# Performance work log

Hardware: AMD Instinct MI355X
Metric: run time of the kernel (lower is better)

The kernel has to match this reference:

```python
import jax, jax.numpy as jnp
import numpy as np

D_MODEL = 2048
D_HEAD = 128
NUM_HEADS = 16
D_LATENT = 512
B, S = 4, 2048


def setup_inputs() -> dict:
    key = jax.random.key(0)
    ks = jax.random.split(key, 11)
    sc = lambda fan_in: 1.0 / np.sqrt(fan_in)
    x = jax.random.normal(ks[0], (B, S, D_MODEL), dtype=jnp.float32)
    # weights stored as [in, out] (transpose of torch nn.Linear.weight)
    W_down = jax.random.uniform(ks[1], (D_MODEL, D_LATENT), jnp.float32, -sc(D_MODEL), sc(D_MODEL))
    b_down = jax.random.uniform(ks[2], (D_LATENT,), jnp.float32, -sc(D_MODEL), sc(D_MODEL))
    W_uk = jax.random.uniform(ks[3], (D_LATENT, D_MODEL), jnp.float32, -sc(D_LATENT), sc(D_LATENT))
    b_uk = jax.random.uniform(ks[4], (D_MODEL,), jnp.float32, -sc(D_LATENT), sc(D_LATENT))
    W_uv = jax.random.uniform(ks[5], (D_LATENT, D_MODEL), jnp.float32, -sc(D_LATENT), sc(D_LATENT))
    b_uv = jax.random.uniform(ks[6], (D_MODEL,), jnp.float32, -sc(D_LATENT), sc(D_LATENT))
    W_q = jax.random.uniform(ks[7], (D_MODEL, NUM_HEADS * D_HEAD), jnp.float32, -sc(D_MODEL), sc(D_MODEL))
    b_q = jax.random.uniform(ks[8], (NUM_HEADS * D_HEAD,), jnp.float32, -sc(D_MODEL), sc(D_MODEL))
    W_o = jax.random.uniform(ks[9], (NUM_HEADS * D_HEAD, D_MODEL), jnp.float32, -sc(NUM_HEADS * D_HEAD), sc(NUM_HEADS * D_HEAD))
    b_o = jax.random.uniform(ks[10], (D_MODEL,), jnp.float32, -sc(NUM_HEADS * D_HEAD), sc(NUM_HEADS * D_HEAD))
    return {"x": x, "W_down": W_down, "b_down": b_down, "W_uk": W_uk, "b_uk": b_uk,
            "W_uv": W_uv, "b_uv": b_uv, "W_q": W_q, "b_q": b_q, "W_o": W_o, "b_o": b_o}


def reference(x, W_down, b_down, W_uk, b_uk, W_uv, b_uv, W_q, b_q, W_o, b_o):
    b, s, _ = x.shape
    latents = x @ W_down + b_down                      # [B,S,L]
    keys = latents @ W_uk + b_uk                       # [B,S,D]
    values = latents @ W_uv + b_uv                     # [B,S,D]
    q = (x @ W_q + b_q).reshape(b, s, NUM_HEADS, D_HEAD).transpose(0, 2, 1, 3)
    k = keys.reshape(b, s, NUM_HEADS, D_HEAD).transpose(0, 2, 1, 3)
    v = values.reshape(b, s, NUM_HEADS, D_HEAD).transpose(0, 2, 1, 3)
    scores = jnp.einsum('bhqd,bhkd->bhqk', q, k) / np.sqrt(D_HEAD).astype(np.float32)
    attn = jax.nn.softmax(scores, axis=-1)
    ctx = jnp.einsum('bhqk,bhkd->bhqd', attn, v)       # [B,H,S,Dh]
    ctx = ctx.transpose(0, 2, 1, 3).reshape(b, s, NUM_HEADS * D_HEAD)
    return ctx @ W_o + b_o
```

## Files before the change

kernel.cpp:

```cpp
#include <hip/hip_runtime.h>

#define D_MODEL 2048
#define D_LATENT 512
#define NUM_HEADS 16
#define D_HEAD 128
#define BATCH 4
#define SEQ 2048
#define MTOK (BATCH*SEQ)

typedef __bf16 bf16_t;
typedef __bf16 bf16x4 __attribute__((ext_vector_type(4)));
typedef __bf16 bf16x8 __attribute__((ext_vector_type(8)));
typedef float  f32x4  __attribute__((ext_vector_type(4)));

__device__ __forceinline__ void load_lds16(const bf16_t* g, bf16_t* l) {
  __builtin_amdgcn_global_load_lds(
      (const __attribute__((address_space(1))) void*)g,
      (__attribute__((address_space(3))) void*)l,
      16, 0, 0);
}

__global__ void convert_f32_bf16_kernel(const float* __restrict__ src,
                                        bf16_t* __restrict__ dst, int n4) {
  int i = blockIdx.x * 256 + threadIdx.x;
  if (i >= n4) return;
  float4 v = *(const float4*)&src[(size_t)i * 4];
  bf16x4 o = { (bf16_t)v.x, (bf16_t)v.y, (bf16_t)v.z, (bf16_t)v.w };
  *(bf16x4*)&dst[(size_t)i * 4] = o;
}

__global__ void transpose_w_kernel(const float* __restrict__ src, bf16_t* __restrict__ dst,
                                   int R, int C) {
  __shared__ __align__(16) bf16_t tile[64][66];
  int rt = blockIdx.y * 64, ct = blockIdx.x * 64;
  int lc = threadIdx.x & 63, lr = threadIdx.x >> 6;
  for (int i = 0; i < 64; i += 4)
    tile[lr + i][lc] = (bf16_t)src[(size_t)(rt + lr + i) * C + ct + lc];
  __syncthreads();
  for (int i = 0; i < 64; i += 4)
    dst[(size_t)(ct + lr + i) * R + rt + lc] = tile[lc][lr + i];
}

__global__ void transpose_v_kernel(const bf16_t* __restrict__ v, bf16_t* __restrict__ vt) {
  __shared__ __align__(16) bf16_t tile[64][66];
  int bh = blockIdx.z; int b = bh >> 4, h = bh & 15;
  int st = blockIdx.x * 64, dt = blockIdx.y * 64;
  int lc = threadIdx.x & 63, lr = threadIdx.x >> 6;
  const bf16_t* src = v + (size_t)b * SEQ * D_MODEL + h * D_HEAD;
  for (int i = 0; i < 64; i += 4)
    tile[lr + i][lc] = src[(size_t)(st + lr + i) * D_MODEL + dt + lc];
  __syncthreads();
  bf16_t* dst = vt + (size_t)bh * D_HEAD * SEQ;
  for (int i = 0; i < 64; i += 4)
    dst[(size_t)(dt + lr + i) * SEQ + st + lc] = tile[lc][lr + i];
}

template<typename OutT>
__global__ __launch_bounds__(256, 2) void gemm_bt_kernel(
    const bf16_t* __restrict__ A, const bf16_t* __restrict__ Wt,
    const float* __restrict__ bias, OutT* __restrict__ C,
    int M, int N, int K, float premul)
{
  __shared__ __align__(16) bf16_t As[128 * 32];
  __shared__ __align__(16) bf16_t Bs[128 * 32];
  int tid = threadIdx.x;
  int lane = tid & 63, wave = tid >> 6;
  int wr = (wave >> 1) * 64, wc = (wave & 1) * 64;
  size_t row0 = (size_t)blockIdx.x * 128, col0 = (size_t)blockIdx.y * 128;
  int lr = lane & 15, quad = lane >> 4, rq = quad * 4;

  f32x4 acc[4][4] = {};

  int srow = wave * 32 + (lane >> 2);
  int scol = ((lane & 3) ^ ((lane >> 3) & 3)) * 8;
  const bf16_t* Ag = A  + (row0 + srow) * K + scol;
  const bf16_t* Bg = Wt + (col0 + srow) * K + scol;
  bf16_t* Asw = As + wave * 1024;
  bf16_t* Bsw = Bs + wave * 1024;

  int rchunk = (quad ^ ((lr >> 1) & 3)) * 8;

  for (int k0 = 0; k0 < K; k0 += 32) {
    __syncthreads();
    load_lds16(Ag,          Asw);
    load_lds16(Ag + 16 * K, Asw + 512);
    load_lds16(Bg,          Bsw);
    load_lds16(Bg + 16 * K, Bsw + 512);
    Ag += 32; Bg += 32;
    __syncthreads();

    bf16x8 af[4], bfr[4];
    #pragma unroll
    for (int mi = 0; mi < 4; ++mi)
      af[mi] = *(const bf16x8*)&As[(wr + mi * 16 + lr) * 32 + rchunk];
    #pragma unroll
    for (int ni = 0; ni < 4; ++ni)
      bfr[ni] = *(const bf16x8*)&Bs[(wc + ni * 16 + lr) * 32 + rchunk];
    #pragma unroll
    for (int mi = 0; mi < 4; ++mi)
      #pragma unroll
      for (int ni = 0; ni < 4; ++ni)
        acc[mi][ni] = __builtin_amdgcn_mfma_f32_16x16x32_bf16(af[mi], bfr[ni], acc[mi][ni], 0, 0, 0);
  }

  #pragma unroll
  for (int ni = 0; ni < 4; ++ni) {
    int col = (int)col0 + wc + ni * 16 + lr;
    float bv = bias[col];
    #pragma unroll
    for (int mi = 0; mi < 4; ++mi) {
      #pragma unroll
      for (int r = 0; r < 4; ++r) {
        size_t row = row0 + wr + mi * 16 + rq + r;
        C[row * N + col] = (OutT)((acc[mi][ni][r] + bv) * premul);
      }
    }
  }
}

__global__ __launch_bounds__(256, 2) void attention_kernel(
    const bf16_t* __restrict__ q, const bf16_t* __restrict__ keys,
    const bf16_t* __restrict__ vt, bf16_t* __restrict__ ctx)
{
  __shared__ __align__(16) bf16_t KP[64 * 128];
  __shared__ __align__(16) bf16_t VS[128 * 64];
  int bh = blockIdx.y; int b = bh >> 4, h = bh & 15;
  int qt = blockIdx.x;
  int tid = threadIdx.x, lane = tid & 63, wave = tid >> 6;
  int lr = lane & 15, quad = lane >> 4, kq = quad * 8, rq = quad * 4;
  int l7 = lr & 7;

  const bf16_t* qg = q    + (size_t)(b * SEQ + qt * 128) * D_MODEL + h * D_HEAD;
  const bf16_t* kg = keys + (size_t)b * SEQ * D_MODEL + h * D_HEAD;
  const bf16_t* vg = vt   + (size_t)bh * D_HEAD * SEQ;

  bf16x8 qf[2][4];
  #pragma unroll
  for (int mi = 0; mi < 2; ++mi)
    #pragma unroll
    for (int ks = 0; ks < 4; ++ks)
      qf[mi][ks] = *(const bf16x8*)&qg[(size_t)(wave*32 + mi*16 + lr) * D_MODEL + ks*32 + kq];

  bf16x8 kreg[4], vreg[4];
  const bf16_t* kp4[4];
  const bf16_t* vp4[4];
  bf16_t* kd4[4];
  bf16_t* vd4[4];
  #pragma unroll
  for (int i = 0; i < 4; ++i) {
    int c = tid + i * 256;
    int r = c >> 4, kc = c & 15;
    kp4[i] = kg + (size_t)r * D_MODEL + kc * 8;
    kd4[i] = &KP[r * 128 + ((kc ^ (r & 7)) * 8)];
    int d = c >> 3, vc = c & 7;
    vp4[i] = vg + (size_t)d * SEQ + vc * 8;
    vd4[i] = &VS[d * 64 + ((vc ^ (d & 7)) * 8)];
  }
  #pragma unroll
  for (int i = 0; i < 4; ++i) {
    kreg[i] = *(const bf16x8*)kp4[i];
    vreg[i] = *(const bf16x8*)vp4[i];
  }

  f32x4 accO[2][8] = {};
  float m2[2]   = {-1e30f, -1e30f};
  float lsum[2] = {0.f, 0.f};

  for (int kt = 0; kt < SEQ/64; ++kt) {
    __syncthreads();
    #pragma unroll
    for (int i = 0; i < 4; ++i) {
      *(bf16x8*)kd4[i] = kreg[i];
      *(bf16x8*)vd4[i] = vreg[i];
    }
    __syncthreads();

    f32x4 sc[2][4] = {};
    #pragma unroll
    for (int ks = 0; ks < 4; ++ks) {
      bf16x8 kf[4];
      #pragma unroll
      for (int ni = 0; ni < 4; ++ni)
        kf[ni] = *(const bf16x8*)&KP[(ni*16 + lr) * 128 + (((ks*4 + quad) ^ l7) * 8)];
      __builtin_amdgcn_s_setprio(1);
      #pragma unroll
      for (int mi = 0; mi < 2; ++mi)
        #pragma unroll
        for (int ni = 0; ni < 4; ++ni)
          sc[mi][ni] = __builtin_amdgcn_mfma_f32_16x16x32_bf16(kf[ni], qf[mi][ks], sc[mi][ni], 0, 0, 0);
      __builtin_amdgcn_s_setprio(0);
    }

    __syncthreads();

    if (kt + 1 < SEQ/64) {
      #pragma unroll
      for (int i = 0; i < 4; ++i) {
        kp4[i] += 64 * D_MODEL;
        vp4[i] += 64;
        kreg[i] = *(const bf16x8*)kp4[i];
        vreg[i] = *(const bf16x8*)vp4[i];
      }
    }

    #pragma unroll
    for (int mi = 0; mi < 2; ++mi) {
      float rm = sc[mi][0][0];
      #pragma unroll
      for (int ni = 0; ni < 4; ++ni)
        #pragma unroll
        for (int r = 0; r < 4; ++r) rm = fmaxf(rm, sc[mi][ni][r]);
      rm = fmaxf(rm, __shfl_xor(rm, 16, 64));
      rm = fmaxf(rm, __shfl_xor(rm, 32, 64));

      if (!__all(rm - m2[mi] <= 8.0f)) {
        float mnew  = fmaxf(m2[mi], rm);
        float alpha = exp2f(m2[mi] - mnew);
        m2[mi] = mnew;
        lsum[mi] *= alpha;
        float ar[4];
        #pragma unroll
        for (int r = 0; r < 4; ++r) ar[r] = __shfl(alpha, rq + r, 16);
        #pragma unroll
        for (int nd = 0; nd < 8; ++nd)
          #pragma unroll
          for (int r = 0; r < 4; ++r) accO[mi][nd][r] *= ar[r];
      }

      float rs = 0.f;
      int prow = wave*32 + mi*16 + lr;
      int pbase = prow * 64;
      int psw = prow & 7;
      #pragma unroll
      for (int ni = 0; ni < 4; ++ni) {
        float p0 = exp2f(sc[mi][ni][0] - m2[mi]);
        float p1 = exp2f(sc[mi][ni][1] - m2[mi]);
        float p2 = exp2f(sc[mi][ni][2] - m2[mi]);
        float p3 = exp2f(sc[mi][ni][3] - m2[mi]);
        rs += (p0 + p1) + (p2 + p3);
        bf16x4 pk = { (bf16_t)p0, (bf16_t)p1, (bf16_t)p2, (bf16_t)p3 };
        *(bf16x4*)&KP[pbase + (((ni*2 + (quad>>1)) ^ psw) * 8) + (quad&1)*4] = pk;
      }
      rs += __shfl_xor(rs, 16, 64);
      rs += __shfl_xor(rs, 32, 64);
      lsum[mi] += rs;
    }


    #pragma unroll
    for (int ks2 = 0; ks2 < 2; ++ks2) {
      bf16x8 pf[2], vf[8];
      #pragma unroll
      for (int mi = 0; mi < 2; ++mi)
        pf[mi] = *(const bf16x8*)&KP[(wave*32 + mi*16 + lr) * 64 + (((ks2*4 + quad) ^ l7) * 8)];
      #pragma unroll
      for (int nd = 0; nd < 8; ++nd)
        vf[nd] = *(const bf16x8*)&VS[(nd*16 + lr) * 64 + (((ks2*4 + quad) ^ l7) * 8)];
      __builtin_amdgcn_s_setprio(1);
      #pragma unroll
      for (int mi = 0; mi < 2; ++mi)
        #pragma unroll
        for (int nd = 0; nd < 8; ++nd)
          accO[mi][nd] = __builtin_amdgcn_mfma_f32_16x16x32_bf16(pf[mi], vf[nd], accO[mi][nd], 0, 0, 0);
      __builtin_amdgcn_s_setprio(0);
    }
  }

  bf16_t* og = ctx + (size_t)(b * SEQ + qt * 128) * D_MODEL + h * D_HEAD;
  #pragma unroll
  for (int mi = 0; mi < 2; ++mi) {
    float inv[4];
    #pragma unroll
    for (int r = 0; r < 4; ++r) inv[r] = 1.0f / __shfl(lsum[mi], rq + r, 16);
    #pragma unroll
    for (int r = 0; r < 4; ++r) {
      int row = wave*32 + mi*16 + rq + r;
      #pragma unroll
      for (int nd = 0; nd < 8; ++nd)
        og[(size_t)row * D_MODEL + nd*16 + lr] = (bf16_t)(accO[mi][nd][r] * inv[r]);
    }
  }
}

extern "C" void kernel_launch(void* const* d_in, const int* in_sizes, int n_in,
                              void* d_out, int out_size, void* d_ws, size_t ws_size,
                              hipStream_t stream) {
  const float* x      = (const float*)d_in[0];
  const float* W_down = (const float*)d_in[1];
  const float* b_down = (const float*)d_in[2];
  const float* W_uk   = (const float*)d_in[3];
  const float* b_uk   = (const float*)d_in[4];
  const float* W_uv   = (const float*)d_in[5];
  const float* b_uv   = (const float*)d_in[6];
  const float* W_q    = (const float*)d_in[7];
  const float* b_q    = (const float*)d_in[8];
  const float* W_o    = (const float*)d_in[9];
  const float* b_o    = (const float*)d_in[10];
  float* out = (float*)d_out;

  char* ws = (char*)d_ws;
  bf16_t* xb      = (bf16_t*)ws;  ws += (size_t)MTOK*D_MODEL*2;
  bf16_t* Wt_down = (bf16_t*)ws;  ws += (size_t)D_LATENT*D_MODEL*2;
  bf16_t* Wt_uk   = (bf16_t*)ws;  ws += (size_t)D_MODEL*D_LATENT*2;
  bf16_t* Wt_uv   = (bf16_t*)ws;  ws += (size_t)D_MODEL*D_LATENT*2;
  bf16_t* Wt_q    = (bf16_t*)ws;  ws += (size_t)D_MODEL*D_MODEL*2;
  bf16_t* Wt_o    = (bf16_t*)ws;  ws += (size_t)D_MODEL*D_MODEL*2;
  bf16_t* lat     = (bf16_t*)ws;  ws += (size_t)MTOK*D_LATENT*2;
  bf16_t* keys    = (bf16_t*)ws;  ws += (size_t)MTOK*D_MODEL*2;
  bf16_t* vals    = (bf16_t*)ws;  ws += (size_t)MTOK*D_MODEL*2;
  bf16_t* qm      = (bf16_t*)ws;  ws += (size_t)MTOK*D_MODEL*2;
  bf16_t* vtm     = (bf16_t*)ws;  ws += (size_t)MTOK*D_MODEL*2;
  bf16_t* ctx     = vals;

  const float cs = 0.0883883476483184f * 1.44269504089f;

  convert_f32_bf16_kernel<<<(MTOK*D_MODEL/4 + 255)/256, 256, 0, stream>>>(x, xb, MTOK*D_MODEL/4);

  transpose_w_kernel<<<dim3(D_LATENT/64, D_MODEL/64), 256, 0, stream>>>(W_down, Wt_down, D_MODEL, D_LATENT);
  transpose_w_kernel<<<dim3(D_MODEL/64, D_LATENT/64), 256, 0, stream>>>(W_uk,   Wt_uk,   D_LATENT, D_MODEL);
  transpose_w_kernel<<<dim3(D_MODEL/64, D_LATENT/64), 256, 0, stream>>>(W_uv,   Wt_uv,   D_LATENT, D_MODEL);
  transpose_w_kernel<<<dim3(D_MODEL/64, D_MODEL/64),  256, 0, stream>>>(W_q,    Wt_q,    D_MODEL,  D_MODEL);
  transpose_w_kernel<<<dim3(D_MODEL/64, D_MODEL/64),  256, 0, stream>>>(W_o,    Wt_o,    D_MODEL,  D_MODEL);

  gemm_bt_kernel<bf16_t><<<dim3(MTOK/128, D_LATENT/128), 256, 0, stream>>>(xb,  Wt_down, b_down, lat,  MTOK, D_LATENT, D_MODEL, 1.0f);
  gemm_bt_kernel<bf16_t><<<dim3(MTOK/128, D_MODEL/128),  256, 0, stream>>>(lat, Wt_uk,   b_uk,   keys, MTOK, D_MODEL,  D_LATENT, 1.0f);
  gemm_bt_kernel<bf16_t><<<dim3(MTOK/128, D_MODEL/128),  256, 0, stream>>>(lat, Wt_uv,   b_uv,   vals, MTOK, D_MODEL,  D_LATENT, 1.0f);
  gemm_bt_kernel<bf16_t><<<dim3(MTOK/128, D_MODEL/128),  256, 0, stream>>>(xb,  Wt_q,    b_q,    qm,   MTOK, D_MODEL,  D_MODEL, cs);

  transpose_v_kernel<<<dim3(SEQ/64, D_HEAD/64, BATCH*NUM_HEADS), 256, 0, stream>>>(vals, vtm);

  attention_kernel<<<dim3(SEQ/128, BATCH*NUM_HEADS), 256, 0, stream>>>(qm, keys, vtm, ctx);

  gemm_bt_kernel<float><<<dim3(MTOK/128, D_MODEL/128), 256, 0, stream>>>(ctx, Wt_o, b_o, out, MTOK, D_MODEL, D_MODEL, 1.0f);
}
```

Before: 614.1 us.

## Double-buffer K/V in LDS with separate P buffer and remap attention grid

Attention now keeps two LDS buffers for K and V plus a separate buffer for P. The next tile is stored into the idle buffer during compute, which cuts the per-iteration barriers from three to one. The launch changes to a 1D grid whose index mapping groups heads that share a query tile, presumably to improve cache locality. LDS use per block grows substantially, which could limit occupancy.

After: 601.3 us. -2.1%, faster.

```diff
diff --git a/kernel.cpp b/kernel.cpp
--- a/kernel.cpp
+++ b/kernel.cpp
@@ -122,10 +122,13 @@
     const bf16_t* __restrict__ q, const bf16_t* __restrict__ keys,
     const bf16_t* __restrict__ vt, bf16_t* __restrict__ ctx)
 {
-  __shared__ __align__(16) bf16_t KP[64 * 128];
-  __shared__ __align__(16) bf16_t VS[128 * 64];
-  int bh = blockIdx.y; int b = bh >> 4, h = bh & 15;
-  int qt = blockIdx.x;
+  __shared__ __align__(16) bf16_t KS[2][64 * 128];
+  __shared__ __align__(16) bf16_t VS[2][128 * 64];
+  __shared__ __align__(16) bf16_t PS[128 * 64];
+  int wg = blockIdx.x;
+  int qt = (wg >> 3) & 15;
+  int bh = (wg & 7) | ((wg >> 7) << 3);
+  int b = bh >> 4, h = bh & 15;
   int tid = threadIdx.x, lane = tid & 63, wave = tid >> 6;
   int lr = lane & 15, quad = lane >> 4, kq = quad * 8, rq = quad * 4;
   int l7 = lr & 7;
@@ -144,36 +147,47 @@
   bf16x8 kreg[4], vreg[4];
   const bf16_t* kp4[4];
   const bf16_t* vp4[4];
-  bf16_t* kd4[4];
-  bf16_t* vd4[4];
+  int kdo[4], vdo[4];
   #pragma unroll
   for (int i = 0; i < 4; ++i) {
     int c = tid + i * 256;
     int r = c >> 4, kc = c & 15;
     kp4[i] = kg + (size_t)r * D_MODEL + kc * 8;
-    kd4[i] = &KP[r * 128 + ((kc ^ (r & 7)) * 8)];
+    kdo[i] = r * 128 + ((kc ^ (r & 7)) * 8);
     int d = c >> 3, vc = c & 7;
     vp4[i] = vg + (size_t)d * SEQ + vc * 8;
-    vd4[i] = &VS[d * 64 + ((vc ^ (d & 7)) * 8)];
-  }
+    vdo[i] = d * 64 + ((vc ^ (d & 7)) * 8);
+  }
+
   #pragma unroll
   for (int i = 0; i < 4; ++i) {
     kreg[i] = *(const bf16x8*)kp4[i];
     vreg[i] = *(const bf16x8*)vp4[i];
   }
+  #pragma unroll
+  for (int i = 0; i < 4; ++i) {
+    *(bf16x8*)&KS[0][kdo[i]] = kreg[i];
+    *(bf16x8*)&VS[0][vdo[i]] = vreg[i];
+  }
+  #pragma unroll
+  for (int i = 0; i < 4; ++i) {
+    kp4[i] += 64 * D_MODEL;
+    vp4[i] += 64;
+    kreg[i] = *(const bf16x8*)kp4[i];
+    vreg[i] = *(const bf16x8*)vp4[i];
+  }
 
   f32x4 accO[2][8] = {};
   float m2[2]   = {-1e30f, -1e30f};
   float lsum[2] = {0.f, 0.f};
 
+  __syncthreads();
+
   for (int kt = 0; kt < SEQ/64; ++kt) {
-    __syncthreads();
-    #pragma unroll
-    for (int i = 0; i < 4; ++i) {
-      *(bf16x8*)kd4[i] = kreg[i];
-      *(bf16x8*)vd4[i] = vreg[i];
-    }
-    __syncthreads();
+    const bf16_t* Kc = KS[kt & 1];
+    const bf16_t* Vc = VS[kt & 1];
+    bf16_t* Kn = KS[(kt & 1) ^ 1];
+    bf16_t* Vn = VS[(kt & 1) ^ 1];
 
     f32x4 sc[2][4] = {};
     #pragma unroll
@@ -181,7 +195,7 @@
       bf16x8 kf[4];
       #pragma unroll
       for (int ni = 0; ni < 4; ++ni)
-        kf[ni] = *(const bf16x8*)&KP[(ni*16 + lr) * 128 + (((ks*4 + quad) ^ l7) * 8)];
+        kf[ni] = *(const bf16x8*)&Kc[(ni*16 + lr) * 128 + (((ks*4 + quad) ^ l7) * 8)];
       __builtin_amdgcn_s_setprio(1);
       #pragma unroll
       for (int mi = 0; mi < 2; ++mi)
@@ -191,9 +205,15 @@
       __builtin_amdgcn_s_setprio(0);
     }
 
-    __syncthreads();
-
     if (kt + 1 < SEQ/64) {
+      #pragma unroll
+      for (int i = 0; i < 4; ++i) {
+        *(bf16x8*)&Kn[kdo[i]] = kreg[i];
+        *(bf16x8*)&VS[(kt & 1) ^ 1][vdo[i]] = vreg[i];
+      }
+    }
+    (void)Vn;
+    if (kt + 2 < SEQ/64) {
       #pragma unroll
       for (int i = 0; i < 4; ++i) {
         kp4[i] += 64 * D_MODEL;
@@ -239,23 +259,22 @@
         float p3 = exp2f(sc[mi][ni][3] - m2[mi]);
         rs += (p0 + p1) + (p2 + p3);
         bf16x4 pk = { (bf16_t)p0, (bf16_t)p1, (bf16_t)p2, (bf16_t)p3 };
-        *(bf16x4*)&KP[pbase + (((ni*2 + (quad>>1)) ^ psw) * 8) + (quad&1)*4] = pk;
+        *(bf16x4*)&PS[pbase + (((ni*2 + (quad>>1)) ^ psw) * 8) + (quad&1)*4] = pk;
       }
       rs += __shfl_xor(rs, 16, 64);
       rs += __shfl_xor(rs, 32, 64);
       lsum[mi] += rs;
     }
 
-
     #pragma unroll
     for (int ks2 = 0; ks2 < 2; ++ks2) {
       bf16x8 pf[2], vf[8];
       #pragma unroll
       for (int mi = 0; mi < 2; ++mi)
-        pf[mi] = *(const bf16x8*)&KP[(wave*32 + mi*16 + lr) * 64 + (((ks2*4 + quad) ^ l7) * 8)];
+        pf[mi] = *(const bf16x8*)&PS[(wave*32 + mi*16 + lr) * 64 + (((ks2*4 + quad) ^ l7) * 8)];
       #pragma unroll
       for (int nd = 0; nd < 8; ++nd)
-        vf[nd] = *(const bf16x8*)&VS[(nd*16 + lr) * 64 + (((ks2*4 + quad) ^ l7) * 8)];
+        vf[nd] = *(const bf16x8*)&Vc[(nd*16 + lr) * 64 + (((ks2*4 + quad) ^ l7) * 8)];
       __builtin_amdgcn_s_setprio(1);
       #pragma unroll
       for (int mi = 0; mi < 2; ++mi)
@@ -264,6 +283,8 @@
           accO[mi][nd] = __builtin_amdgcn_mfma_f32_16x16x32_bf16(pf[mi], vf[nd], accO[mi][nd], 0, 0, 0);
       __builtin_amdgcn_s_setprio(0);
     }
+
+    __syncthreads();
   }
 
   bf16_t* og = ctx + (size_t)(b * SEQ + qt * 128) * D_MODEL + h * D_HEAD;
@@ -329,7 +350,7 @@
 
   transpose_v_kernel<<<dim3(SEQ/64, D_HEAD/64, BATCH*NUM_HEADS), 256, 0, stream>>>(vals, vtm);
 
-  attention_kernel<<<dim3(SEQ/128, BATCH*NUM_HEADS), 256, 0, stream>>>(qm, keys, vtm, ctx);
+  attention_kernel<<<1024, 256, 0, stream>>>(qm, keys, vtm, ctx);
 
   gemm_bt_kernel<float><<<dim3(MTOK/128, D_MODEL/128), 256, 0, stream>>>(ctx, Wt_o, b_o, out, MTOK, D_MODEL, D_MODEL, 1.0f);
 }
```
